# Optimization experiments

Measured on AMD Instinct MI355X. Metric: run time of the kernel, lower is better.

The kernel has to match this reference:

```python
import jax, jax.numpy as jnp
import numpy as np

N, C, H, W = 32, 128, 96, 96
K = 64  # num_clusters
EPS = 1e-12

def _l2norm(v, axis):
    # matches torch F.normalize: v / max(||v||, eps)
    n = jnp.sqrt(jnp.sum(v * v, axis=axis, keepdims=True))
    return v / jnp.maximum(n, EPS)

def setup_inputs() -> dict:
    key = jax.random.key(0)
    ks = jax.random.split(key, 5)
    return {
        "x": jax.random.normal(ks[0], (N, C, H, W), dtype=jnp.float32),
        "conv_w": jax.random.normal(ks[1], (K, C), dtype=jnp.float32) * 0.1,
        "centroids": jax.random.uniform(ks[2], (K, C), dtype=jnp.float32),
        "proj_w": jax.random.normal(ks[3], (C, K * C), dtype=jnp.float32) * 0.02,
        "proj_b": jax.random.normal(ks[4], (C,), dtype=jnp.float32) * 0.01,
    }

def reference(x, conv_w, centroids, proj_w, proj_b):
    n, c = x.shape[:2]
    x = _l2norm(x, axis=1)                       # normalize_input over channels
    xf = x.reshape(n, c, -1)                     # [N, C, HW]
    # 1x1 conv == per-pixel matmul: [N, K, HW]
    logits = jnp.einsum('kc,nch->nkh', conv_w, xf)
    soft = jax.nn.softmax(logits, axis=1)        # softmax over clusters
    # fused VLAD: sum_h a_{nkh} (x_{nch} - c_{kc})
    vlad = jnp.einsum('nkh,nch->nkc', soft, xf) \
         - soft.sum(axis=-1)[:, :, None] * centroids[None]
    vlad = _l2norm(vlad, axis=2)                 # intra-normalization
    vlad = vlad.reshape(n, -1)                   # [N, K*C]
    vlad = _l2norm(vlad, axis=1)
    return vlad @ proj_w.T + proj_b              # [N, C]
```

## Files before the change

kernel.cpp:

```cpp
#include <hip/hip_runtime.h>
#include <hip/hip_bf16.h>

typedef float f32x16 __attribute__((ext_vector_type(16)));
typedef short short8 __attribute__((ext_vector_type(8)));

#define N_IMG 32
#define C_CH  128
#define HW    9216
#define K_CL  64
#define EPSF  1e-12f

#define BPI   24
#define PPB   384
#define NIT   3

#define WS_VLAD 0
#define WS_ASUM (N_IMG*K_CL*C_CH)
#define WS_ZERO (WS_ASUM + N_IMG*K_CL)
#define WS_PART WS_ZERO
#define NPART   (N_IMG*BPI)
#define WS_ASP  (WS_PART + NPART*K_CL*C_CH/2)
#define WS_STORE_TOT (WS_ASP + NPART*K_CL)

__device__ __forceinline__ unsigned short bfb(float f) {
    __hip_bfloat16 h = __float2bfloat16(f);
    return *reinterpret_cast<unsigned short*>(&h);
}
__device__ __forceinline__ float b2f(unsigned short s) {
    return __uint_as_float(((unsigned)s) << 16);
}

__global__ void k_zero(float* __restrict__ p, int cnt) {
    int i = blockIdx.x * blockDim.x + threadIdx.x;
    if (i < cnt) p[i] = 0.f;
}

__global__ __launch_bounds__(256, 3) void k_fused8(
    const float* __restrict__ x, const float* __restrict__ conv_w,
    float* __restrict__ vlad, float* __restrict__ asum,
    unsigned short* __restrict__ part, float* __restrict__ aspart, int use_part)
{
    __shared__ __align__(16) char cw_lds[64 * 256];
    __shared__ __align__(16) char s_lds [64 * 256];
    __shared__ __align__(16) char x_lds [128 * 128];
    __shared__ __align__(16) float invt[128];

    const int t  = threadIdx.x;
    const int w  = t >> 6;
    const int l  = t & 63;
    const int lp = l & 31;
    const int h  = l >> 5;
    const int n    = blockIdx.x / BPI;
    const int pblk = (blockIdx.x % BPI) * PPB;

    #pragma unroll
    for (int r = 0; r < 16; ++r) {
        int e  = t + 256 * r;
        int k  = e >> 6;
        int c2 = (e & 63) << 1;
        unsigned pa = (unsigned)bfb(conv_w[k * C_CH + c2]) |
                      ((unsigned)bfb(conv_w[k * C_CH + c2 + 1]) << 16);
        int addr = (((k << 8) | (c2 << 1)) ^ ((k & 7) << 4));
        *reinterpret_cast<unsigned*>(cw_lds + addr) = pa;
    }

    f32x16 va0, va1;
    #pragma unroll
    for (int r = 0; r < 16; ++r) { va0[r] = 0.f; va1[r] = 0.f; }
    float asum_acc = 0.f;

    const int p  = w * 32 + lp;
    const int q  = p & 63;
    const int myhalf = w >> 1;
    const int ks  = t >> 2;
    const int st4 = t & 3;
    const int hb  = h << 10;
    const float* xbase = x + (size_t)n * C_CH * HW;

    const int swzL = (lp & 7) << 4;
    const int hx   = h << 4;
    const int bA0  = (lp << 8)        | (hx ^ swzL);
    const int bA1  = ((32 + lp) << 8) | (hx ^ swzL);
    const int cB   = 32 * w + lp;
    const int swzC = (cB & 7) << 4;
    const int bXf  = (cB << 7) | (hx ^ swzC);
    int baseS[4];
    #pragma unroll
    for (int j = 0; j < 4; ++j)
        baseS[j] = (((p << 1) ^ ((j + 4 * h) << 4))) + hb;

    for (int it = 0; it < NIT; ++it) {
        const float* xp = xbase + pblk + it * 128 + p;

        float ss = 0.f;
        short8 xb[8];
        #pragma unroll
        for (int s = 0; s < 8; ++s) {
            float xv[8];
            #pragma unroll
            for (int i = 0; i < 8; ++i)
                xv[i] = xp[(size_t)(16 * s + 8 * h + i) * HW];
            #pragma unroll
            for (int i = 0; i < 8; ++i) ss += xv[i] * xv[i];
            #pragma unroll
            for (int i = 0; i < 8; ++i) xb[s][i] = (short)bfb(xv[i]);
        }
        ss += __shfl_xor(ss, 32);
        const float scn = 1.f / fmaxf(sqrtf(ss), EPSF);

        if (it == 0) __syncthreads();

        f32x16 d0, d1;
        #pragma unroll
        for (int r = 0; r < 16; ++r) { d0[r] = 0.f; d1[r] = 0.f; }
        #pragma unroll
        for (int s = 0; s < 8; ++s) {
            short8 a0 = *reinterpret_cast<const short8*>(cw_lds + (bA0 ^ (s << 5)));
            short8 a1 = *reinterpret_cast<const short8*>(cw_lds + (bA1 ^ (s << 5)));
            d0 = __builtin_amdgcn_mfma_f32_32x32x16_bf16(a0, xb[s], d0, 0, 0, 0);
            d1 = __builtin_amdgcn_mfma_f32_32x32x16_bf16(a1, xb[s], d1, 0, 0, 0);
        }

        __syncthreads();

        float sm = 0.f;
        #pragma unroll
        for (int r = 0; r < 16; ++r) {
            float e0 = __expf(d0[r] * scn); sm += e0;
            float e1 = __expf(d1[r] * scn); sm += e1;
            const int imm = ((r & 3) + 8 * (r >> 2)) << 8;
            *reinterpret_cast<short*>(s_lds + (baseS[r & 3] + imm))        = (short)bfb(e0);
            *reinterpret_cast<short*>(s_lds + (baseS[r & 3] + imm + 8192)) = (short)bfb(e1);
        }
        sm += __shfl_xor(sm, 32);
        const float inv = 1.f / sm;
        invt[p] = inv;
        const float sc2 = scn * inv;

        if (myhalf == 0) {
            #pragma unroll
            for (int j = 0; j < 8; ++j) {
                const int bx_ = (((q << 1) ^ (j << 4))) + hb;
                #pragma unroll
                for (int s = 0; s < 8; ++s)
                    *reinterpret_cast<short*>(x_lds + (bx_ + ((16 * s + j) << 7))) =
                        (short)bfb(b2f((unsigned short)xb[s][j]) * sc2);
            }
        }
        __syncthreads();
        #pragma unroll
        for (int sp = 0; sp < 4; ++sp) {
            short8 bf = *reinterpret_cast<const short8*>(x_lds + (bXf ^ (sp << 5)));
            short8 s0 = *reinterpret_cast<const short8*>(s_lds + (bA0 ^ (sp << 5)));
            short8 s1 = *reinterpret_cast<const short8*>(s_lds + (bA1 ^ (sp << 5)));
            va0 = __builtin_amdgcn_mfma_f32_32x32x16_bf16(s0, bf, va0, 0, 0, 0);
            va1 = __builtin_amdgcn_mfma_f32_32x32x16_bf16(s1, bf, va1, 0, 0, 0);
        }
        __syncthreads();

        if (myhalf == 1) {
            #pragma unroll
            for (int j = 0; j < 8; ++j) {
                const int bx_ = (((q << 1) ^ (j << 4))) + hb;
                #pragma unroll
                for (int s = 0; s < 8; ++s)
                    *reinterpret_cast<short*>(x_lds + (bx_ + ((16 * s + j) << 7))) =
                        (short)bfb(b2f((unsigned short)xb[s][j]) * sc2);
            }
        }
        __syncthreads();
        #pragma unroll
        for (int sp = 0; sp < 4; ++sp) {
            short8 bf = *reinterpret_cast<const short8*>(x_lds + (bXf ^ (sp << 5)));
            short8 s0 = *reinterpret_cast<const short8*>(s_lds + ((bA0 ^ (sp << 5)) + 128));
            short8 s1 = *reinterpret_cast<const short8*>(s_lds + ((bA1 ^ (sp << 5)) + 128));
            va0 = __builtin_amdgcn_mfma_f32_32x32x16_bf16(s0, bf, va0, 0, 0, 0);
            va1 = __builtin_amdgcn_mfma_f32_32x32x16_bf16(s1, bf, va1, 0, 0, 0);
        }

        {
            const int rowb = ks << 8;
            const int swz  = (ks & 7) << 4;
            const float* ivp = invt + st4 * 32;
            float a = 0.f;
            #pragma unroll
            for (int g = 0; g < 4; ++g) {
                int off = st4 * 64 + g * 16;
                short8 u = *reinterpret_cast<const short8*>(s_lds + ((rowb | off) ^ swz));
                float4 ia = *reinterpret_cast<const float4*>(ivp + g * 8);
                float4 ib = *reinterpret_cast<const float4*>(ivp + g * 8 + 4);
                a += b2f((unsigned short)u[0]) * ia.x + b2f((unsigned short)u[1]) * ia.y +
                     b2f((unsigned short)u[2]) * ia.z + b2f((unsigned short)u[3]) * ia.w;
                a += b2f((unsigned short)u[4]) * ib.x + b2f((unsigned short)u[5]) * ib.y +
                     b2f((unsigned short)u[6]) * ib.z + b2f((unsigned short)u[7]) * ib.w;
            }
            asum_acc += a;
        }
    }

    if (use_part) {
        unsigned short* pb_ = part + (size_t)blockIdx.x * (K_CL * C_CH) + cB;
        #pragma unroll
        for (int r = 0; r < 16; ++r) {
            const int kr = (r & 3) + 8 * (r >> 2) + 4 * h;
            pb_[(kr)      * C_CH] = bfb(va0[r]);
            pb_[(32 + kr) * C_CH] = bfb(va1[r]);
        }
        float v = asum_acc;
        v += __shfl_xor(v, 1);
        v += __shfl_xor(v, 2);
        if (st4 == 0) aspart[blockIdx.x * K_CL + ks] = v;
    } else {
        float* vb = vlad + (size_t)n * K_CL * C_CH;
        #pragma unroll
        for (int r = 0; r < 16; ++r) {
            const int kr = (r & 3) + 8 * (r >> 2) + 4 * h;
            atomicAdd(vb + (kr)      * C_CH + cB, va0[r]);
            atomicAdd(vb + (32 + kr) * C_CH + cB, va1[r]);
        }
        float v = asum_acc;
        v += __shfl_xor(v, 1);
        v += __shfl_xor(v, 2);
        if (st4 == 0) atomicAdd(asum + n * K_CL + ks, v);
    }
}

__global__ void k_rows_part(float* __restrict__ vlad, const unsigned short* __restrict__ part,
                            const float* __restrict__ aspart,
                            const float* __restrict__ cent)
{
    const int bx = blockIdx.x;
    const int n = bx >> 6, k = bx & 63;
    const int c = threadIdx.x;
    const int b0 = n * BPI;
    float v = 0.f, a = 0.f;
    #pragma unroll
    for (int b = 0; b < BPI; ++b) {
        v += b2f(part[(size_t)(b0 + b) * (K_CL * C_CH) + k * C_CH + c]);
        a += aspart[(b0 + b) * K_CL + k];
    }
    v -= a * cent[k * C_CH + c];
    float ssq = v * v;
    #pragma unroll
    for (int m = 32; m >= 1; m >>= 1) ssq += __shfl_xor(ssq, m);
    __shared__ float sb[2];
    if ((threadIdx.x & 63) == 0) sb[threadIdx.x >> 6] = ssq;
    __syncthreads();
    float tot = sb[0] + sb[1];
    float sc = 1.f / fmaxf(sqrtf(tot), EPSF);
    vlad[((size_t)n * K_CL + k) * C_CH + c] = v * sc;
}

__global__ void k_rows(float* __restrict__ vlad, const float* __restrict__ asum,
                       const float* __restrict__ cent)
{
    const int bx = blockIdx.x;
    const int n = bx >> 6, k = bx & 63;
    const int c = threadIdx.x;
    float a = asum[n * K_CL + k];
    size_t idx = ((size_t)n * K_CL + k) * C_CH + c;
    float v = vlad[idx] - a * cent[k * C_CH + c];
    float ssq = v * v;
    #pragma unroll
    for (int m = 32; m >= 1; m >>= 1) ssq += __shfl_xor(ssq, m);
    __shared__ float sb[2];
    if ((threadIdx.x & 63) == 0) sb[threadIdx.x >> 6] = ssq;
    __syncthreads();
    float tot = sb[0] + sb[1];
    float sc = 1.f / fmaxf(sqrtf(tot), EPSF);
    vlad[idx] = v * sc;
}

__global__ __launch_bounds__(256) void k_proj3(
    const float* __restrict__ vlad, const float* __restrict__ pw,
    const float* __restrict__ pbias, float* __restrict__ out)
{
    const int j  = blockIdx.x;
    const int n0 = blockIdx.y << 2;
    const int t  = threadIdx.x;
    const float4* wp = (const float4*)(pw + (size_t)j * (K_CL * C_CH));
    float4 wr[8];
    #pragma unroll
    for (int r = 0; r < 8; ++r) wr[r] = wp[t + 256 * r];
    __shared__ float sb[4], sb2[4];
    const float bias = pbias[j];
    #pragma unroll
    for (int u = 0; u < 4; ++u) {
        const int n = n0 + u;
        const float4* vp = (const float4*)(vlad + (size_t)n * (K_CL * C_CH));
        float s = 0.f, nn = 0.f;
        #pragma unroll
        for (int r = 0; r < 8; ++r) {
            float4 a = vp[t + 256 * r];
            s  += a.x * wr[r].x + a.y * wr[r].y + a.z * wr[r].z + a.w * wr[r].w;
            nn += a.x * a.x + a.y * a.y + a.z * a.z + a.w * a.w;
        }
        #pragma unroll
        for (int m = 32; m >= 1; m >>= 1) {
            s  += __shfl_xor(s, m);
            nn += __shfl_xor(nn, m);
        }
        if ((t & 63) == 0) { sb[t >> 6] = s; sb2[t >> 6] = nn; }
        __syncthreads();
        if (t == 0) {
            float tot = sb[0] + sb[1] + sb[2] + sb[3];
            float tss = sb2[0] + sb2[1] + sb2[2] + sb2[3];
            float inv = 1.f / fmaxf(sqrtf(tss), EPSF);
            out[n * C_CH + j] = tot * inv + bias;
        }
        __syncthreads();
    }
}

extern "C" void kernel_launch(void* const* d_in, const int* in_sizes, int n_in,
                              void* d_out, int out_size, void* d_ws, size_t ws_size,
                              hipStream_t stream)
{
    const float* x      = (const float*)d_in[0];
    const float* conv_w = (const float*)d_in[1];
    const float* cent   = (const float*)d_in[2];
    const float* pw     = (const float*)d_in[3];
    const float* pbias  = (const float*)d_in[4];
    float* out = (float*)d_out;
    float* ws  = (float*)d_ws;

    float* vlad            = ws + WS_VLAD;
    float* asum            = ws + WS_ASUM;
    unsigned short* part   = (unsigned short*)(ws + WS_PART);
    float* aspart          = ws + WS_ASP;

    const int use_part = (ws_size >= (size_t)WS_STORE_TOT * sizeof(float)) ? 1 : 0;

    if (!use_part) {
        hipLaunchKernelGGL(k_zero, dim3((WS_ZERO + 255) / 256), dim3(256), 0, stream,
                           ws, WS_ZERO);
    }
    hipLaunchKernelGGL(k_fused8, dim3(N_IMG * BPI), dim3(256), 0, stream,
                       x, conv_w, vlad, asum, part, aspart, use_part);
    if (use_part) {
        hipLaunchKernelGGL(k_rows_part, dim3(N_IMG * K_CL), dim3(C_CH), 0, stream,
                           vlad, part, aspart, cent);
    } else {
        hipLaunchKernelGGL(k_rows, dim3(N_IMG * K_CL), dim3(C_CH), 0, stream,
                           vlad, asum, cent);
    }
    hipLaunchKernelGGL(k_proj3, dim3(C_CH, N_IMG / 4), dim3(256), 0, stream,
                       vlad, pw, pbias, out);
}
```

Baseline: 57.53 us.

## Restructure fused VLAD kernel into 64-pixel tiles with coalesced prefetched x staging

The fused assignment/aggregation kernel now processes 64-pixel tiles over six iterations instead of 128-pixel tiles over three. x is loaded with coalesced float4 reads into a bf16 LDS tile, and the next tile is prefetched into registers while the current one is computed. Each wave pair now computes half the clusters, with the softmax denominator combined through shared memory. Normalization is folded into the soft-assignment weights rather than into rescaled x, so the x tile is used unscaled and the asum accumulation is weighted by the per-pixel norm instead. This is meant to remove the strided scalar global loads and the two-phase x_lds rewrite, at the cost of more barriers per pixel and a norm computed from bf16-rounded x.

```diff
diff --git a/kernel.cpp b/kernel.cpp
--- a/kernel.cpp
+++ b/kernel.cpp
@@ -12,7 +12,7 @@
 
 #define BPI   24
 #define PPB   384
-#define NIT   3
+#define NHALF 6
 
 #define WS_VLAD 0
 #define WS_ASUM (N_IMG*K_CL*C_CH)
@@ -35,15 +35,16 @@
     if (i < cnt) p[i] = 0.f;
 }
 
-__global__ __launch_bounds__(256, 3) void k_fused8(
+__global__ __launch_bounds__(256, 3) void k_fused9(
     const float* __restrict__ x, const float* __restrict__ conv_w,
     float* __restrict__ vlad, float* __restrict__ asum,
     unsigned short* __restrict__ part, float* __restrict__ aspart, int use_part)
 {
     __shared__ __align__(16) char cw_lds[64 * 256];
-    __shared__ __align__(16) char s_lds [64 * 256];
-    __shared__ __align__(16) char x_lds [128 * 128];
-    __shared__ __align__(16) float invt[128];
+    __shared__ __align__(16) char s_lds [64 * 128];
+    __shared__ __align__(16) char xs_lds[128 * 128];
+    __shared__ __align__(16) float smpart[2][64];
+    __shared__ __align__(16) float normt[64];
 
     const int t  = threadIdx.x;
     const int w  = t >> 6;
@@ -69,132 +70,138 @@
     for (int r = 0; r < 16; ++r) { va0[r] = 0.f; va1[r] = 0.f; }
     float asum_acc = 0.f;
 
-    const int p  = w * 32 + lp;
-    const int q  = p & 63;
-    const int myhalf = w >> 1;
-    const int ks  = t >> 2;
-    const int st4 = t & 3;
-    const int hb  = h << 10;
+    const int kh   = w >> 1;
+    const int p    = (w & 1) * 32 + lp;
+    const int ks   = t >> 2;
+    const int st4  = t & 3;
     const float* xbase = x + (size_t)n * C_CH * HW;
+
+    const int px4 = (t & 15) << 2;
+    const int c0  = t >> 4;
+    const int tswz = (c0 & 7) << 4;
 
     const int swzL = (lp & 7) << 4;
     const int hx   = h << 4;
-    const int bA0  = (lp << 8)        | (hx ^ swzL);
-    const int bA1  = ((32 + lp) << 8) | (hx ^ swzL);
+    const int bCW  = ((kh * 32 + lp) << 8) | (hx ^ swzL);
     const int cB   = 32 * w + lp;
-    const int swzC = (cB & 7) << 4;
-    const int bXf  = (cB << 7) | (hx ^ swzC);
-    int baseS[4];
-    #pragma unroll
-    for (int j = 0; j < 4; ++j)
-        baseS[j] = (((p << 1) ^ ((j + 4 * h) << 4))) + hb;
-
-    for (int it = 0; it < NIT; ++it) {
-        const float* xp = xbase + pblk + it * 128 + p;
-
+    const int bXf  = (cB << 7) | (hx ^ swzL);
+    const int bS0  = (lp << 7)        | (hx ^ swzL);
+    const int bS1  = ((32 + lp) << 7) | (hx ^ swzL);
+    const int p2   = p << 1;
+
+    {
+        const float* xsrc = xbase + pblk + px4;
+        float4 v[8];
+        #pragma unroll
+        for (int j = 0; j < 8; ++j)
+            v[j] = *reinterpret_cast<const float4*>(xsrc + (size_t)(c0 + 16 * j) * HW);
+        #pragma unroll
+        for (int j = 0; j < 8; ++j) {
+            int c = c0 + 16 * j;
+            uint2 pk;
+            pk.x = (unsigned)bfb(v[j].x) | ((unsigned)bfb(v[j].y) << 16);
+            pk.y = (unsigned)bfb(v[j].z) | ((unsigned)bfb(v[j].w) << 16);
+            *reinterpret_cast<uint2*>(xs_lds + ((c << 7) | ((px4 << 1) ^ tswz))) = pk;
+        }
+    }
+    __syncthreads();
+
+    for (int it = 0; it < NHALF; ++it) {
         float ss = 0.f;
         short8 xb[8];
         #pragma unroll
-        for (int s = 0; s < 8; ++s) {
-            float xv[8];
+        for (int s8 = 0; s8 < 8; ++s8) {
             #pragma unroll
-            for (int i = 0; i < 8; ++i)
-                xv[i] = xp[(size_t)(16 * s + 8 * h + i) * HW];
+            for (int i = 0; i < 8; ++i) {
+                const int c = 16 * s8 + 8 * h + i;
+                short v = *reinterpret_cast<const short*>(
+                    xs_lds + ((c << 7) | (p2 ^ (i << 4))));
+                float f = b2f((unsigned short)v);
+                ss += f * f;
+                xb[s8][i] = v;
+            }
+        }
+        ss += __shfl_xor(ss, 32);
+        const float nrm = fmaxf(sqrtf(ss), EPSF);
+        const float scn = 1.f / nrm;
+
+        float4 v[8];
+        if (it + 1 < NHALF) {
+            const float* xsrc = xbase + pblk + (it + 1) * 64 + px4;
             #pragma unroll
-            for (int i = 0; i < 8; ++i) ss += xv[i] * xv[i];
+            for (int j = 0; j < 8; ++j)
+                v[j] = *reinterpret_cast<const float4*>(xsrc + (size_t)(c0 + 16 * j) * HW);
+        }
+
+        f32x16 d;
+        #pragma unroll
+        for (int r = 0; r < 16; ++r) d[r] = 0.f;
+        #pragma unroll
+        for (int s8 = 0; s8 < 8; ++s8) {
+            short8 a = *reinterpret_cast<const short8*>(cw_lds + (bCW ^ (s8 << 5)));
+            d = __builtin_amdgcn_mfma_f32_32x32x16_bf16(a, xb[s8], d, 0, 0, 0);
+        }
+
+        float e[16];
+        float sm = 0.f;
+        #pragma unroll
+        for (int r = 0; r < 16; ++r) { e[r] = __expf(d[r] * scn); sm += e[r]; }
+        sm += __shfl_xor(sm, 32);
+        if (h == 0) smpart[kh][p] = sm;
+        __syncthreads();
+
+        const float inv = 1.f / (smpart[0][p] + smpart[1][p]);
+        const float esc = inv * scn;
+        #pragma unroll
+        for (int r = 0; r < 16; ++r) {
+            const int kr = (r & 3) + 8 * (r >> 2) + 4 * h;
+            const int k  = kh * 32 + kr;
+            *reinterpret_cast<short*>(
+                s_lds + ((k << 7) | (p2 ^ (((r & 3) + 4 * h) << 4)))) =
+                (short)bfb(e[r] * esc);
+        }
+        if (h == 0 && kh == 0) normt[p] = nrm;
+        __syncthreads();
+
+        #pragma unroll
+        for (int sp = 0; sp < 4; ++sp) {
+            short8 bf = *reinterpret_cast<const short8*>(xs_lds + (bXf ^ (sp << 5)));
+            short8 s0 = *reinterpret_cast<const short8*>(s_lds  + (bS0 ^ (sp << 5)));
+            short8 s1 = *reinterpret_cast<const short8*>(s_lds  + (bS1 ^ (sp << 5)));
+            va0 = __builtin_amdgcn_mfma_f32_32x32x16_bf16(s0, bf, va0, 0, 0, 0);
+            va1 = __builtin_amdgcn_mfma_f32_32x32x16_bf16(s1, bf, va1, 0, 0, 0);
+        }
+
+        {
+            const int rowb = ks << 7;
+            const int swz  = (ks & 7) << 4;
+            const float* np_ = normt + st4 * 16;
+            float a = 0.f;
             #pragma unroll
-            for (int i = 0; i < 8; ++i) xb[s][i] = (short)bfb(xv[i]);
-        }
-        ss += __shfl_xor(ss, 32);
-        const float scn = 1.f / fmaxf(sqrtf(ss), EPSF);
-
-        if (it == 0) __syncthreads();
-
-        f32x16 d0, d1;
-        #pragma unroll
-        for (int r = 0; r < 16; ++r) { d0[r] = 0.f; d1[r] = 0.f; }
-        #pragma unroll
-        for (int s = 0; s < 8; ++s) {
-            short8 a0 = *reinterpret_cast<const short8*>(cw_lds + (bA0 ^ (s << 5)));
-            short8 a1 = *reinterpret_cast<const short8*>(cw_lds + (bA1 ^ (s << 5)));
-            d0 = __builtin_amdgcn_mfma_f32_32x32x16_bf16(a0, xb[s], d0, 0, 0, 0);
-            d1 = __builtin_amdgcn_mfma_f32_32x32x16_bf16(a1, xb[s], d1, 0, 0, 0);
-        }
-
-        __syncthreads();
-
-        float sm = 0.f;
-        #pragma unroll
-        for (int r = 0; r < 16; ++r) {
-            float e0 = __expf(d0[r] * scn); sm += e0;
-            float e1 = __expf(d1[r] * scn); sm += e1;
-            const int imm = ((r & 3) + 8 * (r >> 2)) << 8;
-            *reinterpret_cast<short*>(s_lds + (baseS[r & 3] + imm))        = (short)bfb(e0);
-            *reinterpret_cast<short*>(s_lds + (baseS[r & 3] + imm + 8192)) = (short)bfb(e1);
-        }
-        sm += __shfl_xor(sm, 32);
-        const float inv = 1.f / sm;
-        invt[p] = inv;
-        const float sc2 = scn * inv;
-
-        if (myhalf == 0) {
+            for (int g = 0; g < 2; ++g) {
+                int off = (st4 << 5) | (g << 4);
+                short8 u = *reinterpret_cast<const short8*>(s_lds + (rowb | (off ^ swz)));
+                float4 na = *reinterpret_cast<const float4*>(np_ + g * 8);
+                float4 nb = *reinterpret_cast<const float4*>(np_ + g * 8 + 4);
+                a += b2f((unsigned short)u[0]) * na.x + b2f((unsigned short)u[1]) * na.y +
+                     b2f((unsigned short)u[2]) * na.z + b2f((unsigned short)u[3]) * na.w;
+                a += b2f((unsigned short)u[4]) * nb.x + b2f((unsigned short)u[5]) * nb.y +
+                     b2f((unsigned short)u[6]) * nb.z + b2f((unsigned short)u[7]) * nb.w;
+            }
+            asum_acc += a;
+        }
+
+        if (it + 1 < NHALF) {
+            __syncthreads();
             #pragma unroll
             for (int j = 0; j < 8; ++j) {
-                const int bx_ = (((q << 1) ^ (j << 4))) + hb;
-                #pragma unroll
-                for (int s = 0; s < 8; ++s)
-                    *reinterpret_cast<short*>(x_lds + (bx_ + ((16 * s + j) << 7))) =
-                        (short)bfb(b2f((unsigned short)xb[s][j]) * sc2);
+                int c = c0 + 16 * j;
+                uint2 pk;
+                pk.x = (unsigned)bfb(v[j].x) | ((unsigned)bfb(v[j].y) << 16);
+                pk.y = (unsigned)bfb(v[j].z) | ((unsigned)bfb(v[j].w) << 16);
+                *reinterpret_cast<uint2*>(xs_lds + ((c << 7) | ((px4 << 1) ^ tswz))) = pk;
             }
-        }
-        __syncthreads();
-        #pragma unroll
-        for (int sp = 0; sp < 4; ++sp) {
-            short8 bf = *reinterpret_cast<const short8*>(x_lds + (bXf ^ (sp << 5)));
-            short8 s0 = *reinterpret_cast<const short8*>(s_lds + (bA0 ^ (sp << 5)));
-            short8 s1 = *reinterpret_cast<const short8*>(s_lds + (bA1 ^ (sp << 5)));
-            va0 = __builtin_amdgcn_mfma_f32_32x32x16_bf16(s0, bf, va0, 0, 0, 0);
-            va1 = __builtin_amdgcn_mfma_f32_32x32x16_bf16(s1, bf, va1, 0, 0, 0);
-        }
-        __syncthreads();
-
-        if (myhalf == 1) {
-            #pragma unroll
-            for (int j = 0; j < 8; ++j) {
-                const int bx_ = (((q << 1) ^ (j << 4))) + hb;
-                #pragma unroll
-                for (int s = 0; s < 8; ++s)
-                    *reinterpret_cast<short*>(x_lds + (bx_ + ((16 * s + j) << 7))) =
-                        (short)bfb(b2f((unsigned short)xb[s][j]) * sc2);
-            }
-        }
-        __syncthreads();
-        #pragma unroll
-        for (int sp = 0; sp < 4; ++sp) {
-            short8 bf = *reinterpret_cast<const short8*>(x_lds + (bXf ^ (sp << 5)));
-            short8 s0 = *reinterpret_cast<const short8*>(s_lds + ((bA0 ^ (sp << 5)) + 128));
-            short8 s1 = *reinterpret_cast<const short8*>(s_lds + ((bA1 ^ (sp << 5)) + 128));
-            va0 = __builtin_amdgcn_mfma_f32_32x32x16_bf16(s0, bf, va0, 0, 0, 0);
-            va1 = __builtin_amdgcn_mfma_f32_32x32x16_bf16(s1, bf, va1, 0, 0, 0);
-        }
-
-        {
-            const int rowb = ks << 8;
-            const int swz  = (ks & 7) << 4;
-            const float* ivp = invt + st4 * 32;
-            float a = 0.f;
-            #pragma unroll
-            for (int g = 0; g < 4; ++g) {
-                int off = st4 * 64 + g * 16;
-                short8 u = *reinterpret_cast<const short8*>(s_lds + ((rowb | off) ^ swz));
-                float4 ia = *reinterpret_cast<const float4*>(ivp + g * 8);
-                float4 ib = *reinterpret_cast<const float4*>(ivp + g * 8 + 4);
-                a += b2f((unsigned short)u[0]) * ia.x + b2f((unsigned short)u[1]) * ia.y +
-                     b2f((unsigned short)u[2]) * ia.z + b2f((unsigned short)u[3]) * ia.w;
-                a += b2f((unsigned short)u[4]) * ib.x + b2f((unsigned short)u[5]) * ib.y +
-                     b2f((unsigned short)u[6]) * ib.z + b2f((unsigned short)u[7]) * ib.w;
-            }
-            asum_acc += a;
+            __syncthreads();
         }
     }
 
@@ -206,10 +213,10 @@
             pb_[(kr)      * C_CH] = bfb(va0[r]);
             pb_[(32 + kr) * C_CH] = bfb(va1[r]);
         }
-        float v = asum_acc;
-        v += __shfl_xor(v, 1);
-        v += __shfl_xor(v, 2);
-        if (st4 == 0) aspart[blockIdx.x * K_CL + ks] = v;
+        float vv = asum_acc;
+        vv += __shfl_xor(vv, 1);
+        vv += __shfl_xor(vv, 2);
+        if (st4 == 0) aspart[blockIdx.x * K_CL + ks] = vv;
     } else {
         float* vb = vlad + (size_t)n * K_CL * C_CH;
         #pragma unroll
@@ -218,10 +225,10 @@
             atomicAdd(vb + (kr)      * C_CH + cB, va0[r]);
             atomicAdd(vb + (32 + kr) * C_CH + cB, va1[r]);
         }
-        float v = asum_acc;
-        v += __shfl_xor(v, 1);
-        v += __shfl_xor(v, 2);
-        if (st4 == 0) atomicAdd(asum + n * K_CL + ks, v);
+        float vv = asum_acc;
+        vv += __shfl_xor(vv, 1);
+        vv += __shfl_xor(vv, 2);
+        if (st4 == 0) atomicAdd(asum + n * K_CL + ks, vv);
     }
 }
 
@@ -335,7 +342,7 @@
         hipLaunchKernelGGL(k_zero, dim3((WS_ZERO + 255) / 256), dim3(256), 0, stream,
                            ws, WS_ZERO);
     }
-    hipLaunchKernelGGL(k_fused8, dim3(N_IMG * BPI), dim3(256), 0, stream,
+    hipLaunchKernelGGL(k_fused9, dim3(N_IMG * BPI), dim3(256), 0, stream,
                        x, conv_w, vlad, asum, part, aspart, use_part);
     if (use_part) {
         hipLaunchKernelGGL(k_rows_part, dim3(N_IMG * K_CL), dim3(C_CH), 0, stream,
```

Result: slower. 91.71 us (+59.4%).
